# Kernel optimization log

Hardware: AMD Instinct MI355X
Metric: run time of the kernel (lower is better)

## Reference

```python
import jax, jax.numpy as jnp
import numpy as np

N = 16384          # batch
K = 4096           # num_neurons per LogicLayer
L = 4              # num_layers
IN0 = 4            # first layer in_dim (= 2*D from cat([x,-x]))
CLASSES = 2
TAU = 1.0


def setup_inputs() -> dict:
    key = jax.random.key(0)
    k1, k2, k3 = jax.random.split(key, 3)
    rng = np.random.default_rng(0)
    x = jax.random.normal(k1, (N, 2), dtype=jnp.float32)
    w0 = jax.random.normal(k2, (K, 16), dtype=jnp.float32)
    ws = jax.random.normal(k3, (L - 1, K, 16), dtype=jnp.float32)
    ia0 = jnp.asarray(rng.integers(0, IN0, size=(K,)), dtype=jnp.int32)
    ib0 = jnp.asarray(rng.integers(0, IN0, size=(K,)), dtype=jnp.int32)
    ia = jnp.asarray(rng.integers(0, K, size=(L - 1, K)), dtype=jnp.int32)
    ib = jnp.asarray(rng.integers(0, K, size=(L - 1, K)), dtype=jnp.int32)
    return dict(x=x, w0=w0, ws=ws, ia0=ia0, ib0=ib0, ia=ia, ib=ib)


def logic_layer(h, w, idx_a, idx_b):
    """Differentiable logic layer (difflogic, training mode).

    out = sum_i softmax(w)_i * op_i(a, b) over the 16 two-input boolean
    functions. All 16 ops are multilinear in (a, b), so the weighted sum
    collapses exactly to c0 + ca*a + cb*b + cab*a*b with per-neuron coeffs.
    """
    p = jax.nn.softmax(w, axis=-1)  # [k, 16]
    a = h[:, idx_a]                 # [N, k]
    b = h[:, idx_b]                 # [N, k]
    ca = p[:, 2] + p[:, 3] + p[:, 6] + p[:, 7] - p[:, 8] - p[:, 9] - p[:, 12] - p[:, 13]
    cb = p[:, 4] + p[:, 5] + p[:, 6] + p[:, 7] - p[:, 8] - p[:, 9] - p[:, 10] - p[:, 11]
    cab = (p[:, 1] - p[:, 2] - p[:, 4] - 2.0 * p[:, 6] - p[:, 7]
           + p[:, 8] + 2.0 * p[:, 9] + p[:, 11] + p[:, 13] - p[:, 14])
    c0 = p[:, 8] + p[:, 9] + p[:, 10] + p[:, 11] + p[:, 12] + p[:, 13] + p[:, 14] + p[:, 15]
    return c0 + ca * a + cb * b + cab * (a * b)


def _model(iv, w0, ws, ia0, ib0, ia, ib):
    h = logic_layer(iv, w0, ia0, ib0)
    for l in range(ws.shape[0]):  # small fixed layer loop
        h = logic_layer(h, ws[l], ia[l], ib[l])
    # GroupSum(class_count=2, tau=1.0)
    return h.reshape(h.shape[0], CLASSES, -1).sum(-1) / TAU


def reference(x, w0, ws, ia0, ib0, ia, ib):
    mx = jnp.concatenate([x, -x], axis=1)  # [N, 4]
    thresh_space = 0.5

    # ---- ti = 0: thresh = 0, flags all zero -> input_values = tx ----
    tx = (mx > 0.0).astype(jnp.float32)
    iv = tx
    rt0 = _model(iv, w0, ws, ia0, ib0, ia, ib)          # [N, 2]
    # flags[n,d,o] = 1 where input_values[n,d] != results[n,0,o]
    flags = (iv[:, :, None] != rt0[:, None, :]).astype(jnp.float32)  # [N, 4, 2]

    # ---- ti = 1 ----
    lastl = jnp.argmax(rt0, axis=1)                      # [N]
    wadj = jnp.where(lastl > 0, thresh_space, -thresh_space)
    thresh = wadj                                        # started from zeros
    tx = (mx > thresh[:, None]).astype(jnp.float32)
    # nested oi-loop writes tx wherever flags[n,d,oi]==0 for any oi
    upd = jnp.any(flags == 0.0, axis=2)                  # [N, 4]
    iv = jnp.where(upd, tx, iv)
    rt1 = _model(iv, w0, ws, ia0, ib0, ia, ib)           # [N, 2]
    return rt1
```

## Files before the change

kernel.cpp:

```cpp
#include <hip/hip_runtime.h>

#define KN 4096
#define NSAMP 16384
#define NNEUR (4 * KN)

__device__ __forceinline__ void coeffs_from_w(const float* __restrict__ w,
                                              float& c0, float& ca, float& cb, float& cab) {
    float m = w[0];
    #pragma unroll
    for (int j = 1; j < 16; ++j) m = fmaxf(m, w[j]);
    float p[16];
    float s = 0.0f;
    #pragma unroll
    for (int j = 0; j < 16; ++j) { p[j] = expf(w[j] - m); s += p[j]; }
    float inv = 1.0f / s;
    #pragma unroll
    for (int j = 0; j < 16; ++j) p[j] *= inv;
    ca  = p[2] + p[3] + p[6] + p[7] - p[8] - p[9] - p[12] - p[13];
    cb  = p[4] + p[5] + p[6] + p[7] - p[8] - p[9] - p[10] - p[11];
    cab = p[1] - p[2] - p[4] - 2.0f*p[6] - p[7] + p[8] + 2.0f*p[9] + p[11] + p[13] - p[14];
    c0  = p[8] + p[9] + p[10] + p[11] + p[12] + p[13] + p[14] + p[15];
}

__global__ __launch_bounds__(256) void compute_coeffs(
    const float* __restrict__ w0, const float* __restrict__ wsG,
    float4* __restrict__ coeffs) {
    int g = blockIdx.x * 256 + threadIdx.x;
    if (g >= NNEUR) return;
    const float* wp = (g < KN) ? (w0 + (size_t)g * 16)
                               : (wsG + (size_t)(g - KN) * 16);
    float w[16];
    const float4* wr = (const float4*)wp;
    float4 v0 = wr[0], v1 = wr[1], v2 = wr[2], v3 = wr[3];
    w[0]=v0.x; w[1]=v0.y; w[2]=v0.z; w[3]=v0.w;
    w[4]=v1.x; w[5]=v1.y; w[6]=v1.z; w[7]=v1.w;
    w[8]=v2.x; w[9]=v2.y; w[10]=v2.z; w[11]=v2.w;
    w[12]=v3.x; w[13]=v3.y; w[14]=v3.z; w[15]=v3.w;
    float c0, ca, cb, cab;
    coeffs_from_w(w, c0, ca, cb, cab);
    coeffs[g] = make_float4(c0, ca, cb, cab);
}

__global__ __launch_bounds__(1024) void build_table(
    const float4* __restrict__ coeffs,
    const int* __restrict__ ia0, const int* __restrict__ ib0,
    const int* __restrict__ ia, const int* __restrict__ ib,
    float* __restrict__ table) {
    __shared__ float h0[KN];
    __shared__ float h1[KN];
    __shared__ float red[2][16];
    const int pat = blockIdx.x;
    const int tid = threadIdx.x;

    #pragma unroll
    for (int i = 0; i < 4; ++i) {
        int k = tid + i * 1024;
        float4 c = coeffs[k];
        float a = (float)((pat >> ia0[k]) & 1);
        float b = (float)((pat >> ib0[k]) & 1);
        h0[k] = c.x + c.y * a + c.z * b + c.w * (a * b);
    }
    __syncthreads();

#define LAYER(L, SRC, DST)                                                    \
    {                                                                         \
        const int* ial = ia + (L) * KN;                                       \
        const int* ibl = ib + (L) * KN;                                       \
        _Pragma("unroll")                                                     \
        for (int i = 0; i < 4; ++i) {                                         \
            int k = tid + i * 1024;                                           \
            float4 c = coeffs[((L) + 1) * KN + k];                            \
            float a = SRC[ial[k]];                                            \
            float b = SRC[ibl[k]];                                            \
            DST[k] = c.x + c.y * a + c.z * b + c.w * (a * b);                 \
        }                                                                     \
        __syncthreads();                                                      \
    }
    LAYER(0, h0, h1)
    LAYER(1, h1, h0)
    LAYER(2, h0, h1)
#undef LAYER

    float s0 = h1[tid] + h1[tid + 1024];
    float s1 = h1[tid + 2048] + h1[tid + 3072];
    #pragma unroll
    for (int off = 32; off > 0; off >>= 1) {
        s0 += __shfl_down(s0, off, 64);
        s1 += __shfl_down(s1, off, 64);
    }
    int wid = tid >> 6, lane = tid & 63;
    if (lane == 0) { red[0][wid] = s0; red[1][wid] = s1; }
    __syncthreads();
    if (tid == 0) {
        float t0 = 0.0f, t1 = 0.0f;
        #pragma unroll
        for (int wq = 0; wq < 16; ++wq) { t0 += red[0][wq]; t1 += red[1][wq]; }
        table[pat * 2 + 0] = t0;
        table[pat * 2 + 1] = t1;
    }
}

__global__ __launch_bounds__(256) void classify(
    const float* __restrict__ x, const float* __restrict__ table_g,
    float* __restrict__ out) {
    __shared__ float table[32];
    if (threadIdx.x < 32) table[threadIdx.x] = table_g[threadIdx.x];
    __syncthreads();
    int n = blockIdx.x * 256 + threadIdx.x;
    if (n >= NSAMP) return;
    float2 xv = ((const float2*)x)[n];
    float mx[4] = { xv.x, xv.y, -xv.x, -xv.y };
    int p0 = 0;
    float ivf[4];
    #pragma unroll
    for (int i = 0; i < 4; ++i) {
        int b = mx[i] > 0.0f;
        ivf[i] = (float)b;
        p0 |= b << i;
    }
    float r0 = table[p0 * 2 + 0];
    float r1 = table[p0 * 2 + 1];
    int lastl = (r1 > r0) ? 1 : 0;
    float thresh = lastl ? 0.5f : -0.5f;
    int p1 = 0;
    #pragma unroll
    for (int i = 0; i < 4; ++i) {
        bool upd = (ivf[i] == r0) || (ivf[i] == r1);
        int bit = upd ? (int)(mx[i] > thresh) : (int)ivf[i];
        p1 |= bit << i;
    }
    float2 o;
    o.x = table[p1 * 2 + 0];
    o.y = table[p1 * 2 + 1];
    ((float2*)out)[n] = o;
}

extern "C" void kernel_launch(void* const* d_in, const int* in_sizes, int n_in,
                              void* d_out, int out_size, void* d_ws, size_t ws_size,
                              hipStream_t stream) {
    const float* x   = (const float*)d_in[0];
    const float* w0  = (const float*)d_in[1];
    const float* wsG = (const float*)d_in[2];
    const int* ia0   = (const int*)d_in[3];
    const int* ib0   = (const int*)d_in[4];
    const int* ia    = (const int*)d_in[5];
    const int* ib    = (const int*)d_in[6];

    float* table   = (float*)d_ws;
    float4* coeffs = (float4*)((char*)d_ws + 128);

    compute_coeffs<<<(NNEUR + 255) / 256, 256, 0, stream>>>(w0, wsG, coeffs);
    build_table<<<16, 1024, 0, stream>>>(coeffs, ia0, ib0, ia, ib, table);
    classify<<<NSAMP / 256, 256, 0, stream>>>(x, table, (float*)d_out);
}
```

Baseline: 18.24 us.

## Fuse coefficient, table and classify kernels into one cooperative launch

Merges the three kernels into a single cooperative kernel of 16 blocks x 1024 threads, using grid-wide syncs between the coefficient, table-building and classification phases. This removes two kernel launch gaps. The softmax drops max-subtraction and uses fast __expf, folding normalization into the four coefficients. That risks overflow for large weights and leaves only 16 blocks for the coefficient and classify phases.

Result: slower. 39.05 us (+114.1%).

```diff
diff --git a/kernel.cpp b/kernel.cpp
--- a/kernel.cpp
+++ b/kernel.cpp
@@ -1,56 +1,47 @@
 #include <hip/hip_runtime.h>
+#include <hip/hip_cooperative_groups.h>
+
+namespace cg = cooperative_groups;
 
 #define KN 4096
 #define NSAMP 16384
-#define NNEUR (4 * KN)
 
-__device__ __forceinline__ void coeffs_from_w(const float* __restrict__ w,
-                                              float& c0, float& ca, float& cb, float& cab) {
-    float m = w[0];
-    #pragma unroll
-    for (int j = 1; j < 16; ++j) m = fmaxf(m, w[j]);
-    float p[16];
-    float s = 0.0f;
-    #pragma unroll
-    for (int j = 0; j < 16; ++j) { p[j] = expf(w[j] - m); s += p[j]; }
-    float inv = 1.0f / s;
-    #pragma unroll
-    for (int j = 0; j < 16; ++j) p[j] *= inv;
-    ca  = p[2] + p[3] + p[6] + p[7] - p[8] - p[9] - p[12] - p[13];
-    cb  = p[4] + p[5] + p[6] + p[7] - p[8] - p[9] - p[10] - p[11];
-    cab = p[1] - p[2] - p[4] - 2.0f*p[6] - p[7] + p[8] + 2.0f*p[9] + p[11] + p[13] - p[14];
-    c0  = p[8] + p[9] + p[10] + p[11] + p[12] + p[13] + p[14] + p[15];
-}
-
-__global__ __launch_bounds__(256) void compute_coeffs(
+__global__ __launch_bounds__(1024) void fused_all(
+    const float* __restrict__ x,
     const float* __restrict__ w0, const float* __restrict__ wsG,
-    float4* __restrict__ coeffs) {
-    int g = blockIdx.x * 256 + threadIdx.x;
-    if (g >= NNEUR) return;
-    const float* wp = (g < KN) ? (w0 + (size_t)g * 16)
-                               : (wsG + (size_t)(g - KN) * 16);
-    float w[16];
-    const float4* wr = (const float4*)wp;
-    float4 v0 = wr[0], v1 = wr[1], v2 = wr[2], v3 = wr[3];
-    w[0]=v0.x; w[1]=v0.y; w[2]=v0.z; w[3]=v0.w;
-    w[4]=v1.x; w[5]=v1.y; w[6]=v1.z; w[7]=v1.w;
-    w[8]=v2.x; w[9]=v2.y; w[10]=v2.z; w[11]=v2.w;
-    w[12]=v3.x; w[13]=v3.y; w[14]=v3.z; w[15]=v3.w;
-    float c0, ca, cb, cab;
-    coeffs_from_w(w, c0, ca, cb, cab);
-    coeffs[g] = make_float4(c0, ca, cb, cab);
-}
-
-__global__ __launch_bounds__(1024) void build_table(
-    const float4* __restrict__ coeffs,
     const int* __restrict__ ia0, const int* __restrict__ ib0,
     const int* __restrict__ ia, const int* __restrict__ ib,
-    float* __restrict__ table) {
+    float4* __restrict__ coeffs, float* __restrict__ table,
+    float* __restrict__ out) {
+    cg::grid_group grid = cg::this_grid();
     __shared__ float h0[KN];
     __shared__ float h1[KN];
     __shared__ float red[2][16];
+    __shared__ float tbl[32];
+    const int tid = threadIdx.x;
     const int pat = blockIdx.x;
-    const int tid = threadIdx.x;
+    const int g = pat * 1024 + tid;
+
+    {
+        const float* wp = (g < KN) ? (w0 + (size_t)g * 16)
+                                   : (wsG + (size_t)(g - KN) * 16);
+        const float4* wr = (const float4*)wp;
+        float4 v0 = wr[0], v1 = wr[1], v2 = wr[2], v3 = wr[3];
+        float e0 = __expf(v0.x), e1 = __expf(v0.y), e2 = __expf(v0.z), e3 = __expf(v0.w);
+        float e4 = __expf(v1.x), e5 = __expf(v1.y), e6 = __expf(v1.z), e7 = __expf(v1.w);
+        float e8 = __expf(v2.x), e9 = __expf(v2.y), e10 = __expf(v2.z), e11 = __expf(v2.w);
+        float e12 = __expf(v3.x), e13 = __expf(v3.y), e14 = __expf(v3.z), e15 = __expf(v3.w);
+        float s = ((e0 + e1) + (e2 + e3)) + ((e4 + e5) + (e6 + e7))
+                + ((e8 + e9) + (e10 + e11)) + ((e12 + e13) + (e14 + e15));
+        float can  = ((e2 + e3) + (e6 + e7)) - ((e8 + e9) + (e12 + e13));
+        float cbn  = ((e4 + e5) + (e6 + e7)) - ((e8 + e9) + (e10 + e11));
+        float cabn = (e1 - e2) - (e4 + e7) - 2.0f * e6 + (e8 + e11) + 2.0f * e9
+                   + (e13 - e14);
+        float c0n  = ((e8 + e9) + (e10 + e11)) + ((e12 + e13) + (e14 + e15));
+        float inv = 1.0f / s;
+        coeffs[g] = make_float4(c0n * inv, can * inv, cbn * inv, cabn * inv);
+    }
+    grid.sync();
 
     #pragma unroll
     for (int i = 0; i < 4; ++i) {
@@ -81,58 +72,56 @@
     LAYER(2, h0, h1)
 #undef LAYER
 
-    float s0 = h1[tid] + h1[tid + 1024];
-    float s1 = h1[tid + 2048] + h1[tid + 3072];
-    #pragma unroll
-    for (int off = 32; off > 0; off >>= 1) {
-        s0 += __shfl_down(s0, off, 64);
-        s1 += __shfl_down(s1, off, 64);
+    {
+        float s0 = h1[tid] + h1[tid + 1024];
+        float s1 = h1[tid + 2048] + h1[tid + 3072];
+        #pragma unroll
+        for (int off = 32; off > 0; off >>= 1) {
+            s0 += __shfl_down(s0, off, 64);
+            s1 += __shfl_down(s1, off, 64);
+        }
+        int wid = tid >> 6, lane = tid & 63;
+        if (lane == 0) { red[0][wid] = s0; red[1][wid] = s1; }
+        __syncthreads();
+        if (tid == 0) {
+            float t0 = 0.0f, t1 = 0.0f;
+            #pragma unroll
+            for (int wq = 0; wq < 16; ++wq) { t0 += red[0][wq]; t1 += red[1][wq]; }
+            table[pat * 2 + 0] = t0;
+            table[pat * 2 + 1] = t1;
+        }
     }
-    int wid = tid >> 6, lane = tid & 63;
-    if (lane == 0) { red[0][wid] = s0; red[1][wid] = s1; }
+    grid.sync();
+
+    if (tid < 32) tbl[tid] = table[tid];
     __syncthreads();
-    if (tid == 0) {
-        float t0 = 0.0f, t1 = 0.0f;
+    {
+        float2 xv = ((const float2*)x)[g];
+        float mx[4] = { xv.x, xv.y, -xv.x, -xv.y };
+        int p0 = 0;
+        float ivf[4];
         #pragma unroll
-        for (int wq = 0; wq < 16; ++wq) { t0 += red[0][wq]; t1 += red[1][wq]; }
-        table[pat * 2 + 0] = t0;
-        table[pat * 2 + 1] = t1;
+        for (int i = 0; i < 4; ++i) {
+            int b = mx[i] > 0.0f;
+            ivf[i] = (float)b;
+            p0 |= b << i;
+        }
+        float r0 = tbl[p0 * 2 + 0];
+        float r1 = tbl[p0 * 2 + 1];
+        int lastl = (r1 > r0) ? 1 : 0;
+        float thresh = lastl ? 0.5f : -0.5f;
+        int p1 = 0;
+        #pragma unroll
+        for (int i = 0; i < 4; ++i) {
+            bool upd = (ivf[i] == r0) || (ivf[i] == r1);
+            int bit = upd ? (int)(mx[i] > thresh) : (int)ivf[i];
+            p1 |= bit << i;
+        }
+        float2 o;
+        o.x = tbl[p1 * 2 + 0];
+        o.y = tbl[p1 * 2 + 1];
+        ((float2*)out)[g] = o;
     }
-}
-
-__global__ __launch_bounds__(256) void classify(
-    const float* __restrict__ x, const float* __restrict__ table_g,
-    float* __restrict__ out) {
-    __shared__ float table[32];
-    if (threadIdx.x < 32) table[threadIdx.x] = table_g[threadIdx.x];
-    __syncthreads();
-    int n = blockIdx.x * 256 + threadIdx.x;
-    if (n >= NSAMP) return;
-    float2 xv = ((const float2*)x)[n];
-    float mx[4] = { xv.x, xv.y, -xv.x, -xv.y };
-    int p0 = 0;
-    float ivf[4];
-    #pragma unroll
-    for (int i = 0; i < 4; ++i) {
-        int b = mx[i] > 0.0f;
-        ivf[i] = (float)b;
-        p0 |= b << i;
-    }
-    float r0 = table[p0 * 2 + 0];
-    float r1 = table[p0 * 2 + 1];
-    int lastl = (r1 > r0) ? 1 : 0;
-    float thresh = lastl ? 0.5f : -0.5f;
-    int p1 = 0;
-    #pragma unroll
-    for (int i = 0; i < 4; ++i) {
-        bool upd = (ivf[i] == r0) || (ivf[i] == r1);
-        int bit = upd ? (int)(mx[i] > thresh) : (int)ivf[i];
-        p1 |= bit << i;
-    }
-    float2 o;
-    o.x = table[p1 * 2 + 0];
-    o.y = table[p1 * 2 + 1];
-    ((float2*)out)[n] = o;
 }
 
 extern "C" void kernel_launch(void* const* d_in, const int* in_sizes, int n_in,
@@ -145,11 +134,14 @@
     const int* ib0   = (const int*)d_in[4];
     const int* ia    = (const int*)d_in[5];
     const int* ib    = (const int*)d_in[6];
+    float* out       = (float*)d_out;
 
     float* table   = (float*)d_ws;
-    float4* coeffs = (float4*)((char*)d_ws + 128);
+    float4* coeffs = (float4*)((char*)d_ws + 256);
 
-    compute_coeffs<<<(NNEUR + 255) / 256, 256, 0, stream>>>(w0, wsG, coeffs);
-    build_table<<<16, 1024, 0, stream>>>(coeffs, ia0, ib0, ia, ib, table);
-    classify<<<NSAMP / 256, 256, 0, stream>>>(x, table, (float*)d_out);
+    void* args[] = { (void*)&x, (void*)&w0, (void*)&wsG,
+                     (void*)&ia0, (void*)&ib0, (void*)&ia, (void*)&ib,
+                     (void*)&coeffs, (void*)&table, (void*)&out };
+    hipLaunchCooperativeKernel((void*)fused_all, dim3(16), dim3(1024),
+                               args, 0, stream);
 }
```
